# Optimization experiments

Hardware: AMD Instinct MI355X
Metric: run time of the kernel (lower is better)

Reference implementation:

```python
import jax, jax.numpy as jnp
import numpy as np

K_CHAINS, N_STATES, ALPHABET, SEQ_LEN = 3, 12, 32, 64


def setup_inputs() -> dict:
    key = jax.random.key(0)
    k0, k1, k2, k3, k4 = jax.random.split(key, 5)
    return {
        "ys": jax.random.randint(k0, (SEQ_LEN,), 0, ALPHABET),
        "transition": jax.random.normal(k1, (K_CHAINS, N_STATES, N_STATES), jnp.float32),
        "emission": jax.random.normal(k2, (K_CHAINS, N_STATES, ALPHABET), jnp.float32),
        "choice": jax.random.normal(k3, (K_CHAINS,), jnp.float32),
        "prior": jax.random.normal(k4, (K_CHAINS, N_STATES), jnp.float32),
    }


def reference(ys, transition, emission, choice, prior):
    K, S = transition.shape[0], transition.shape[1]
    c = jax.nn.log_softmax(choice)                  # (K,)
    t = jax.nn.log_softmax(transition, axis=-1)     # (K,S,S)
    e = jax.nn.log_softmax(emission, axis=-1)       # (K,S,A)
    p = jax.nn.log_softmax(prior, axis=-1)          # (K,S)

    # enumerate expanded state space: tuples (s_1..s_K, i) -> N = S^K * K rows
    grids = jnp.meshgrid(*([jnp.arange(S)] * K + [jnp.arange(K)]), indexing="ij")
    tbl = jnp.stack(grids, -1).reshape(-1, K + 1)   # (N, K+1)
    states = tbl[:, :K]                             # (N, K) chain states
    chain = tbl[:, K]                               # (N,)   active chain index

    # transition matrix A[m, n] = logprob(old expanded state n -> new expanded state m)
    onehot = jax.nn.one_hot(chain, K, dtype=bool)   # (N, K)
    eq = states[:, None, :] == states[None, :, :]   # (N_new, N_old, K)
    valid = jnp.where(onehot[:, None, :], True, eq).all(-1)  # non-active chains unchanged
    s_new = jnp.take_along_axis(states, chain[:, None], axis=1)[:, 0]  # (N,) new state of active chain
    s_old = states[:, chain]                        # (N_old, N_new): old state at chain[m]
    t_term = t[chain[None, :], s_old, s_new[None, :]]  # (N_old, N_new)
    Amat = c[chain][:, None] + t_term.T + jnp.where(valid, 0.0, -jnp.inf)  # (N_new, N_old)

    # emission table B[m, y] = e[chain[m], state of active chain, y]
    B = e[chain, s_new]                             # (N, A)

    # initial alpha: sum_j p[j, s_j] + c[i]
    alpha0 = p[jnp.arange(K)[None, :], states].sum(-1) + c[chain]  # (N,)

    def step(alpha, y):
        alpha = B[:, y] + jax.nn.logsumexp(alpha[None, :] + Amat, axis=-1)
        return alpha, None

    alpha, _ = jax.lax.scan(step, alpha0, ys)
    return jax.nn.logsumexp(alpha)
```

## Files before the change

kernel.cpp:

```cpp
#include <hip/hip_runtime.h>
#include <math.h>

#define KC 3
#define S 12
#define SS 1728
#define AB 32
#define TLEN 64
#define NTHREADS 896
#define NWAVES 14
#define NACT 864
#define LN2F 0.69314718055994530942f

__global__ __launch_bounds__(NTHREADS, 4)
void hmm_fwd_kernel(const int* __restrict__ ys,
                    const float* __restrict__ transition,
                    const float* __restrict__ emission,
                    const float* __restrict__ choice,
                    const float* __restrict__ prior,
                    float* __restrict__ out)
{
    __shared__ __align__(16) float APL[KC][SS];
    __shared__ __align__(16) float BETA[SS];
    __shared__ __align__(16) float ECt[KC][AB][16];
    __shared__ float T_s[KC][S][S];
    __shared__ float p_lin[KC][S];
    __shared__ float c_lin[KC];
    __shared__ int   ys_s[TLEN];
    __shared__ float wsum[NWAVES];

    const int tid = threadIdx.x;

    if (tid < TLEN) ys_s[tid] = ys[tid];

    if (tid == 0) {
        float m = fmaxf(fmaxf(choice[0], choice[1]), choice[2]);
        float e0 = __expf(choice[0]-m), e1 = __expf(choice[1]-m), e2 = __expf(choice[2]-m);
        float inv = 1.f / (e0+e1+e2);
        c_lin[0] = e0*inv; c_lin[1] = e1*inv; c_lin[2] = e2*inv;
    }
    if (tid >= 1 && tid < 1 + KC) {
        int k = tid - 1;
        float m = -INFINITY;
        #pragma unroll
        for (int i = 0; i < S; ++i) m = fmaxf(m, prior[k*S + i]);
        float ev[S]; float s = 0.f;
        #pragma unroll
        for (int i = 0; i < S; ++i) { ev[i] = __expf(prior[k*S + i] - m); s += ev[i]; }
        float inv = 1.f / s;
        #pragma unroll
        for (int i = 0; i < S; ++i) p_lin[k][i] = ev[i] * inv;
    }
    if (tid >= 64 && tid < 64 + KC*S) {
        int r = tid - 64;
        int k = r / S, i = r % S;
        const float* row = transition + (k*S + i)*S;
        float m = -INFINITY;
        #pragma unroll
        for (int j = 0; j < S; ++j) m = fmaxf(m, row[j]);
        float ev[S]; float s = 0.f;
        #pragma unroll
        for (int j = 0; j < S; ++j) { ev[j] = __expf(row[j] - m); s += ev[j]; }
        float inv = 1.f / s;
        #pragma unroll
        for (int j = 0; j < S; ++j) T_s[k][i][j] = ev[j] * inv;
    }
    if (tid >= 128 && tid < 128 + KC*S) {
        int r = tid - 128;
        int k = r / S, sj = r % S;
        float cm = fmaxf(fmaxf(choice[0], choice[1]), choice[2]);
        float ce = __expf(choice[k]-cm) /
                   (__expf(choice[0]-cm) + __expf(choice[1]-cm) + __expf(choice[2]-cm));
        const float* row = emission + (k*S + sj)*AB;
        float m = -INFINITY;
        #pragma unroll
        for (int a = 0; a < AB; ++a) m = fmaxf(m, row[a]);
        float ev[AB]; float s = 0.f;
        #pragma unroll
        for (int a = 0; a < AB; ++a) { ev[a] = __expf(row[a] - m); s += ev[a]; }
        float inv = ce / s;
        const int slot = (sj / 6) * 8 + (sj % 6);
        #pragma unroll
        for (int a = 0; a < AB; ++a) ECt[k][a][slot] = ev[a] * inv;
    }
    __syncthreads();

    const bool act = tid < NACT;
    const int ct = act ? tid : (NACT - 1);
    const int sl = ct >> 1;
    const int h  = ct & 1;
    const int sk = sl / 144;
    const int q  = sl % 144;
    const int qh = q / 12, ql = q % 12;

    const int rdb = (sk == 0) ? q : (sk == 1) ? 144*qh + ql : 12*q;
    const int wstr = (sk == 0) ? 144 : (sk == 1) ? 12 : 1;
    const int wbas = rdb + wstr * 6 * h;
    float* const wap = &APL[sk][wbas];
    const float* const ecp = &ECt[sk][0][8*h];

    float Trg[S][6];
    if (act) {
        #pragma unroll
        for (int i = 0; i < S; ++i) {
            #pragma unroll
            for (int m = 0; m < 6; ++m) Trg[i][m] = T_s[sk][i][6*h + m];
        }
    }

    if (act) {
        const int sA = 2*tid;
        const int a0 = sA/144, b0 = (sA/12)%12, c0 = sA%12;
        const float pp = p_lin[0][a0]*p_lin[1][b0];
        const float pA = pp*p_lin[2][c0], pB = pp*p_lin[2][c0+1];
        #pragma unroll
        for (int k = 0; k < KC; ++k) {
            float2 v; v.x = pA*c_lin[k]; v.y = pB*c_lin[k];
            *reinterpret_cast<float2*>(&APL[k][sA]) = v;
        }
    }
    __syncthreads();

    float logR = 0.f, invR = 1.f;
    const int s2p = 2*tid;

    #pragma unroll 1
    for (int t = 0; t < TLEN; ++t) {
        const int y = ys_s[t];

        if (act) {
            float2 a0 = *reinterpret_cast<const float2*>(&APL[0][s2p]);
            float2 a1 = *reinterpret_cast<const float2*>(&APL[1][s2p]);
            float2 a2 = *reinterpret_cast<const float2*>(&APL[2][s2p]);
            float2 b;
            b.x = (a0.x + a1.x + a2.x) * invR;
            b.y = (a0.y + a1.y + a2.y) * invR;
            *reinterpret_cast<float2*>(&BETA[s2p]) = b;
        }
        __syncthreads();

        float acc0=0.f, acc1=0.f, acc2=0.f, acc3=0.f, acc4=0.f, acc5=0.f;
        if (act) {
            float4 e03 = *reinterpret_cast<const float4*>(&ecp[y*16]);
            float2 e45 = *reinterpret_cast<const float2*>(&ecp[y*16 + 4]);

            float bv[S];
            if (sk == 0) {
                #pragma unroll
                for (int i = 0; i < S; ++i) bv[i] = BETA[rdb + 144*i];
            } else if (sk == 1) {
                #pragma unroll
                for (int i = 0; i < S; ++i) bv[i] = BETA[rdb + 12*i];
            } else {
                float4 r0 = *reinterpret_cast<const float4*>(&BETA[rdb + 0]);
                float4 r1 = *reinterpret_cast<const float4*>(&BETA[rdb + 4]);
                float4 r2 = *reinterpret_cast<const float4*>(&BETA[rdb + 8]);
                bv[0]=r0.x; bv[1]=r0.y; bv[2] =r0.z; bv[3] =r0.w;
                bv[4]=r1.x; bv[5]=r1.y; bv[6] =r1.z; bv[7] =r1.w;
                bv[8]=r2.x; bv[9]=r2.y; bv[10]=r2.z; bv[11]=r2.w;
            }

            #pragma unroll
            for (int i = 0; i < S; ++i) {
                const float bb = bv[i];
                acc0 = __builtin_fmaf(bb, Trg[i][0], acc0);
                acc1 = __builtin_fmaf(bb, Trg[i][1], acc1);
                acc2 = __builtin_fmaf(bb, Trg[i][2], acc2);
                acc3 = __builtin_fmaf(bb, Trg[i][3], acc3);
                acc4 = __builtin_fmaf(bb, Trg[i][4], acc4);
                acc5 = __builtin_fmaf(bb, Trg[i][5], acc5);
            }
            acc0 *= e03.x; acc1 *= e03.y; acc2 *= e03.z;
            acc3 *= e03.w; acc4 *= e45.x; acc5 *= e45.y;

            if (sk == 2) {
                if (h == 0) {
                    *reinterpret_cast<float4*>(&wap[0]) = make_float4(acc0, acc1, acc2, acc3);
                    *reinterpret_cast<float2*>(&wap[4]) = make_float2(acc4, acc5);
                } else {
                    *reinterpret_cast<float2*>(&wap[0]) = make_float2(acc0, acc1);
                    *reinterpret_cast<float4*>(&wap[2]) = make_float4(acc2, acc3, acc4, acc5);
                }
            } else {
                wap[0*wstr] = acc0; wap[1*wstr] = acc1; wap[2*wstr] = acc2;
                wap[3*wstr] = acc3; wap[4*wstr] = acc4; wap[5*wstr] = acc5;
            }
        }

        if ((t & 7) == 7) {
            float part = acc0 + acc1 + acc2 + acc3 + acc4 + acc5;
            part += __shfl_xor(part, 32); part += __shfl_xor(part, 16);
            part += __shfl_xor(part, 8);  part += __shfl_xor(part, 4);
            part += __shfl_xor(part, 2);  part += __shfl_xor(part, 1);
            if ((tid & 63) == 0) wsum[tid >> 6] = part;
        }
        __syncthreads();

        if ((t & 7) == 7 && t < TLEN-1) {
            float R = 0.f;
            #pragma unroll
            for (int w = 0; w < NWAVES; ++w) R += wsum[w];
            invR = __builtin_amdgcn_rcpf(R);
            logR += __log2f(R);
        } else {
            invR = 1.f;
        }
    }

    if (tid == 0) {
        float R = 0.f;
        #pragma unroll
        for (int w = 0; w < NWAVES; ++w) R += wsum[w];
        out[0] = LN2F * (__log2f(R) + logR);
    }
}

extern "C" void kernel_launch(void* const* d_in, const int* in_sizes, int n_in,
                              void* d_out, int out_size, void* d_ws, size_t ws_size,
                              hipStream_t stream) {
    const int*   ys         = (const int*)  d_in[0];
    const float* transition = (const float*)d_in[1];
    const float* emission   = (const float*)d_in[2];
    const float* choice     = (const float*)d_in[3];
    const float* prior      = (const float*)d_in[4];
    float* out = (float*)d_out;

    hipLaunchKernelGGL(hmm_fwd_kernel, dim3(1), dim3(NTHREADS), 0, stream,
                       ys, transition, emission, choice, prior, out);
}
```

Measured before the change: 60.34 us.

## Store beta in three transposed copies so every chain reads contiguous float4

The summed beta vector is now written into three shared arrays, each laid out so the active chain's index is innermost. The matvec phase can then read all 12 inputs with three float4 loads instead of strided scalar loads for chains 0 and 1. This trades extra scalar shared-memory stores in the beta phase for vectorized, divergence-free reads in the hot phase. The transition table is also padded to 16 columns and read through volatile pointers for all threads, including inactive ones.

```diff
diff --git a/kernel.cpp b/kernel.cpp
--- a/kernel.cpp
+++ b/kernel.cpp
@@ -20,9 +20,9 @@
                     float* __restrict__ out)
 {
     __shared__ __align__(16) float APL[KC][SS];
-    __shared__ __align__(16) float BETA[SS];
+    __shared__ __align__(16) float B0[SS], B1[SS], B2[SS];
     __shared__ __align__(16) float ECt[KC][AB][16];
-    __shared__ float T_s[KC][S][S];
+    __shared__ __align__(16) float T_s[KC][S][16];
     __shared__ float p_lin[KC][S];
     __shared__ float c_lin[KC];
     __shared__ int   ys_s[TLEN];
@@ -62,7 +62,7 @@
         for (int j = 0; j < S; ++j) { ev[j] = __expf(row[j] - m); s += ev[j]; }
         float inv = 1.f / s;
         #pragma unroll
-        for (int j = 0; j < S; ++j) T_s[k][i][j] = ev[j] * inv;
+        for (int j = 0; j < S; ++j) T_s[k][i][(j/6)*8 + (j%6)] = ev[j] * inv;
     }
     if (tid >= 128 && tid < 128 + KC*S) {
         int r = tid - 128;
@@ -92,49 +92,54 @@
     const int q  = sl % 144;
     const int qh = q / 12, ql = q % 12;
 
-    const int rdb = (sk == 0) ? q : (sk == 1) ? 144*qh + ql : 12*q;
+    const float* const rp = ((sk == 0) ? B0 : (sk == 1) ? B1 : B2) + 12*q;
     const int wstr = (sk == 0) ? 144 : (sk == 1) ? 12 : 1;
-    const int wbas = rdb + wstr * 6 * h;
+    const int wbas = ((sk == 0) ? q : (sk == 1) ? 144*qh + ql : 12*q) + wstr*6*h;
     float* const wap = &APL[sk][wbas];
     const float* const ecp = &ECt[sk][0][8*h];
 
+    const int n  = 2 * ct;
+    const int s0 = n / 144, s1 = (n / 12) % 12, s2 = n % 12;
+    const int w1b = 144*s0 + 12*s2 + s1;
+    const int w0b = 144*s1 + 12*s2 + s0;
+
     float Trg[S][6];
+    {
+        #pragma unroll
+        for (int i = 0; i < S; ++i) {
+            volatile const float* tv = &T_s[sk][i][8*h];
+            Trg[i][0] = tv[0]; Trg[i][1] = tv[1]; Trg[i][2] = tv[2];
+            Trg[i][3] = tv[3]; Trg[i][4] = tv[4]; Trg[i][5] = tv[5];
+        }
+    }
+
     if (act) {
-        #pragma unroll
-        for (int i = 0; i < S; ++i) {
-            #pragma unroll
-            for (int m = 0; m < 6; ++m) Trg[i][m] = T_s[sk][i][6*h + m];
-        }
-    }
-
-    if (act) {
-        const int sA = 2*tid;
-        const int a0 = sA/144, b0 = (sA/12)%12, c0 = sA%12;
-        const float pp = p_lin[0][a0]*p_lin[1][b0];
-        const float pA = pp*p_lin[2][c0], pB = pp*p_lin[2][c0+1];
+        const float pp = p_lin[0][s0] * p_lin[1][s1];
+        const float pA = pp * p_lin[2][s2], pB = pp * p_lin[2][s2+1];
         #pragma unroll
         for (int k = 0; k < KC; ++k) {
-            float2 v; v.x = pA*c_lin[k]; v.y = pB*c_lin[k];
-            *reinterpret_cast<float2*>(&APL[k][sA]) = v;
+            float2 v; v.x = pA * c_lin[k]; v.y = pB * c_lin[k];
+            *reinterpret_cast<float2*>(&APL[k][n]) = v;
         }
     }
     __syncthreads();
 
     float logR = 0.f, invR = 1.f;
-    const int s2p = 2*tid;
 
     #pragma unroll 1
     for (int t = 0; t < TLEN; ++t) {
         const int y = ys_s[t];
 
         if (act) {
-            float2 a0 = *reinterpret_cast<const float2*>(&APL[0][s2p]);
-            float2 a1 = *reinterpret_cast<const float2*>(&APL[1][s2p]);
-            float2 a2 = *reinterpret_cast<const float2*>(&APL[2][s2p]);
+            float2 a0 = *reinterpret_cast<const float2*>(&APL[0][n]);
+            float2 a1 = *reinterpret_cast<const float2*>(&APL[1][n]);
+            float2 a2 = *reinterpret_cast<const float2*>(&APL[2][n]);
             float2 b;
             b.x = (a0.x + a1.x + a2.x) * invR;
             b.y = (a0.y + a1.y + a2.y) * invR;
-            *reinterpret_cast<float2*>(&BETA[s2p]) = b;
+            *reinterpret_cast<float2*>(&B2[n]) = b;
+            B1[w1b] = b.x; B1[w1b + 12] = b.y;
+            B0[w0b] = b.x; B0[w0b + 12] = b.y;
         }
         __syncthreads();
 
@@ -143,21 +148,13 @@
             float4 e03 = *reinterpret_cast<const float4*>(&ecp[y*16]);
             float2 e45 = *reinterpret_cast<const float2*>(&ecp[y*16 + 4]);
 
+            float4 r0 = *reinterpret_cast<const float4*>(&rp[0]);
+            float4 r1 = *reinterpret_cast<const float4*>(&rp[4]);
+            float4 r2 = *reinterpret_cast<const float4*>(&rp[8]);
             float bv[S];
-            if (sk == 0) {
-                #pragma unroll
-                for (int i = 0; i < S; ++i) bv[i] = BETA[rdb + 144*i];
-            } else if (sk == 1) {
-                #pragma unroll
-                for (int i = 0; i < S; ++i) bv[i] = BETA[rdb + 12*i];
-            } else {
-                float4 r0 = *reinterpret_cast<const float4*>(&BETA[rdb + 0]);
-                float4 r1 = *reinterpret_cast<const float4*>(&BETA[rdb + 4]);
-                float4 r2 = *reinterpret_cast<const float4*>(&BETA[rdb + 8]);
-                bv[0]=r0.x; bv[1]=r0.y; bv[2] =r0.z; bv[3] =r0.w;
-                bv[4]=r1.x; bv[5]=r1.y; bv[6] =r1.z; bv[7] =r1.w;
-                bv[8]=r2.x; bv[9]=r2.y; bv[10]=r2.z; bv[11]=r2.w;
-            }
+            bv[0]=r0.x; bv[1]=r0.y; bv[2] =r0.z; bv[3] =r0.w;
+            bv[4]=r1.x; bv[5]=r1.y; bv[6] =r1.z; bv[7] =r1.w;
+            bv[8]=r2.x; bv[9]=r2.y; bv[10]=r2.z; bv[11]=r2.w;
 
             #pragma unroll
             for (int i = 0; i < S; ++i) {
```

Result: slower. 67.83 us (+12.4%).
